# Kernel optimization log

Measured on AMD Instinct MI355X. Metric: run time of the kernel, lower is better.

The kernel has to match this reference:

```python
import jax, jax.numpy as jnp
import numpy as np

BATCH, DIM, L, N = 2, 4096, 2048, 16


def setup_inputs() -> dict:
    key = jax.random.key(0)
    ks = jax.random.split(key, 8)
    ri = lambda k, shape: jax.random.randint(k, shape, -127, 128).astype(jnp.int32)
    return {
        "u": ri(ks[0], (BATCH, DIM, L)),
        "dt": ri(ks[1], (BATCH, DIM, L)),
        "B": ri(ks[2], (BATCH, N, L)),
        "C": ri(ks[3], (BATCH, N, L)),
        "z": ri(ks[4], (BATCH, DIM, L)),
        "A_log": ri(ks[5], (DIM, N)),
        "D": ri(ks[6], (DIM,)),
        "dt_bias": ri(ks[7], (DIM,)),
        # per-tensor absmax-style scales (scalar fp32 buffers in QSScan)
        "u_scale": jnp.float32(0.01),
        "dt_scale": jnp.float32(0.004),
        "A_scale": jnp.float32(0.02),
        "B_scale": jnp.float32(0.02),
        "C_scale": jnp.float32(0.02),
        "z_scale": jnp.float32(0.02),
        "D_scale": jnp.float32(0.01),
        "dt_bias_scale": jnp.float32(0.02),
    }


def reference(u, dt, B, C, z, A_log, D, dt_bias,
              u_scale, dt_scale, A_scale, B_scale, C_scale,
              z_scale, D_scale, dt_bias_scale):
    # Dequantize INT8 operands (fused in the CUDA kernel)
    u_f = u.astype(jnp.float32) * u_scale                         # [b,d,l]
    delta = dt.astype(jnp.float32) * dt_scale \
        + (dt_bias.astype(jnp.float32) * dt_bias_scale)[None, :, None]
    delta = jax.nn.softplus(delta)                                # delta_softplus=True
    A = -jnp.exp(A_log.astype(jnp.float32) * A_scale)             # [d,n]
    B_f = B.astype(jnp.float32) * B_scale                         # [b,n,l]
    C_f = C.astype(jnp.float32) * C_scale                         # [b,n,l]

    # time-major inputs for the sequential scan
    xs = (jnp.moveaxis(delta, -1, 0),   # [l,b,d]
          jnp.moveaxis(u_f, -1, 0),     # [l,b,d]
          jnp.moveaxis(B_f, -1, 0),     # [l,b,n]
          jnp.moveaxis(C_f, -1, 0))     # [l,b,n]
    x0 = jnp.zeros((u.shape[0], u.shape[1], A.shape[1]), jnp.float32)  # [b,d,n]

    def step(x, ins):
        d_t, u_t, b_t, c_t = ins
        dA = jnp.exp(d_t[..., None] * A)                          # [b,d,n]
        x = dA * x + (d_t * u_t)[..., None] * b_t[:, None, :]     # ZOH-style discretization
        y_t = jnp.einsum('bdn,bn->bd', x, c_t)
        return x, y_t

    _, ys = jax.lax.scan(step, x0, xs)                            # [l,b,d]
    y = jnp.moveaxis(ys, 0, -1)                                   # [b,d,l]
    y = y + (D.astype(jnp.float32) * D_scale)[None, :, None] * u_f
    z_f = z.astype(jnp.float32) * z_scale
    return y * z_f * jax.nn.sigmoid(z_f)                          # gate: y * silu(z)
```

## Files before the change

### kernel.cpp

```cpp
#include <hip/hip_runtime.h>


#define LOG2E 1.44269504088896340736f
#define LN2F  0.69314718055994530942f

constexpr int BATCH = 2;
constexpr int DIM   = 4096;
constexpr int LSEQ  = 2048;
constexpr int NST   = 16;
constexpr int SCANS = BATCH * DIM;
constexpr int K     = 64;
constexpr int LC    = LSEQ / K;
constexpr int SPB   = 256;
constexpr int NSG   = SCANS / SPB;

__device__ __forceinline__ float softplus_f(float x) {
    float e = __builtin_amdgcn_exp2f(x * LOG2E);
    return __builtin_amdgcn_logf(1.f + e) * LN2F;
}

__device__ __forceinline__ int pack8(int4 v) {
    return (v.x & 255) | ((v.y & 255) << 8) | ((v.z & 255) << 16) | ((v.w & 255) << 24);
}

#define LOAD_A2()                                                              \
    float A2[NST];                                                             \
    {                                                                          \
        const int4* ap = (const int4*)(A_log + d * NST);                       \
        int4 a0 = ap[0], a1 = ap[1], a2 = ap[2], a3 = ap[3];                   \
        const int ai[NST] = {a0.x,a0.y,a0.z,a0.w, a1.x,a1.y,a1.z,a1.w,         \
                             a2.x,a2.y,a2.z,a2.w, a3.x,a3.y,a3.z,a3.w};        \
        _Pragma("unroll")                                                      \
        for (int n = 0; n < NST; ++n)                                          \
            A2[n] = -__builtin_amdgcn_exp2f((float)ai[n] * (A_s * LOG2E)) * LOG2E; \
    }

#define STEP4(q, bt, ct)                                                       \
    {                                                                          \
        const float4 Bq = *(const float4*)((bt) + 4 * (q));                    \
        const float4 Cq = *(const float4*)((ct) + 4 * (q));                    \
        x[4*(q)+0] = __builtin_fmaf(__builtin_amdgcn_exp2f(A2[4*(q)+0] * delta), x[4*(q)+0], w * Bq.x); \
        y = __builtin_fmaf(x[4*(q)+0], Cq.x, y);                               \
        x[4*(q)+1] = __builtin_fmaf(__builtin_amdgcn_exp2f(A2[4*(q)+1] * delta), x[4*(q)+1], w * Bq.y); \
        y = __builtin_fmaf(x[4*(q)+1], Cq.y, y);                               \
        x[4*(q)+2] = __builtin_fmaf(__builtin_amdgcn_exp2f(A2[4*(q)+2] * delta), x[4*(q)+2], w * Bq.z); \
        y = __builtin_fmaf(x[4*(q)+2], Cq.z, y);                               \
        x[4*(q)+3] = __builtin_fmaf(__builtin_amdgcn_exp2f(A2[4*(q)+3] * delta), x[4*(q)+3], w * Bq.w); \
        y = __builtin_fmaf(x[4*(q)+3], Cq.w, y);                               \
    }

#define STEP4B(q, bt)                                                          \
    {                                                                          \
        const float4 Bq = *(const float4*)((bt) + 4 * (q));                    \
        x[4*(q)+0] = __builtin_fmaf(__builtin_amdgcn_exp2f(A2[4*(q)+0] * delta), x[4*(q)+0], w * Bq.x); \
        x[4*(q)+1] = __builtin_fmaf(__builtin_amdgcn_exp2f(A2[4*(q)+1] * delta), x[4*(q)+1], w * Bq.y); \
        x[4*(q)+2] = __builtin_fmaf(__builtin_amdgcn_exp2f(A2[4*(q)+2] * delta), x[4*(q)+2], w * Bq.z); \
        x[4*(q)+3] = __builtin_fmaf(__builtin_amdgcn_exp2f(A2[4*(q)+3] * delta), x[4*(q)+3], w * Bq.w); \
    }

__global__ __launch_bounds__(256, 4) void qs_phase1(
    const int* __restrict__ u,  const int* __restrict__ dt,
    const int* __restrict__ Bm, const int* __restrict__ A_log,
    const int* __restrict__ dt_bias,
    const float* __restrict__ u_sp, const float* __restrict__ dt_sp,
    const float* __restrict__ A_sp, const float* __restrict__ B_sp,
    const float* __restrict__ dtb_sp,
    float* __restrict__ Sbuf, float* __restrict__ Xbuf)
{
    const int tid = threadIdx.x;
    const int cg  = blockIdx.x >> 5;
    const int sg  = blockIdx.x & 31;
    const int scan = sg * SPB + tid;
    const int d  = scan & (DIM - 1);
    const int bb = sg >> 4;

    __shared__ int   sud[256 * 17];
    __shared__ float tB[LC * 20];

    const float u_s = *u_sp, dt_s = *dt_sp, A_s = *A_sp, B_s = *B_sp, dtb_s = *dtb_sp;
    LOAD_A2();
    const float dtb = (float)dt_bias[d] * dtb_s;

    const int lc8 = tid >> 3, lo8 = tid & 7;
    const int in0 = sg * SPB * LSEQ + cg * LC;
    const int kB  = tid & 31, nB0 = tid >> 5;
    const int bcol = tid * 68;

#pragma unroll
    for (int p = 0; p < 8; ++p) {
        const int col = p * 32 + lc8;
        const int ga  = in0 + col * LSEQ + 4 * lo8;
        sud[col * 17 + lo8]     = pack8(*(const int4*)(u  + ga));
        sud[col * 17 + 8 + lo8] = pack8(*(const int4*)(dt + ga));
    }
#pragma unroll
    for (int j2 = 0; j2 < 2; ++j2) {
        const int n = nB0 + 8 * j2;
        tB[kB * 20 + n] = (float)Bm[(bb * NST + n) * LSEQ + cg * LC + kB];
    }
    __syncthreads();

    float x[NST];
#pragma unroll
    for (int n = 0; n < NST; ++n) x[n] = 0.f;
    float S = 0.f;

    const signed char* sc = (const signed char*)sud;
#pragma unroll 4
    for (int k = 0; k < LC; ++k) {
        const float uf    = (float)sc[bcol + k] * u_s;
        const float delta = softplus_f((float)sc[bcol + 32 + k] * dt_s + dtb);
        const float w     = delta * uf * B_s;
        S += delta;
        const float* bt = &tB[k * 20];
        STEP4B(0, bt); STEP4B(1, bt); STEP4B(2, bt); STEP4B(3, bt);
    }

    Sbuf[cg * SCANS + scan] = S;
    float4* Xo = (float4*)(Xbuf + (cg * SCANS + scan) * NST);
#pragma unroll
    for (int q = 0; q < 4; ++q)
        Xo[q] = make_float4(x[4*q], x[4*q+1], x[4*q+2], x[4*q+3]);
}

__global__ __launch_bounds__(256) void qs_combine(
    const int* __restrict__ A_log, const float* __restrict__ A_sp,
    const float* __restrict__ Sbuf, float* __restrict__ Xbuf)
{
    const int idx  = blockIdx.x * 256 + threadIdx.x;
    const int scan = idx >> 4, n = idx & 15;
    const int d    = scan & (DIM - 1);
    const float A2 = -__builtin_amdgcn_exp2f(
        (float)A_log[d * NST + n] * ((*A_sp) * LOG2E)) * LOG2E;
    float x = 0.f;
#pragma unroll 8
    for (int c = 0; c < K; ++c) {
        const int off = c * (SCANS * NST) + idx;
        const float Xe = Xbuf[off];
        const float P  = __builtin_amdgcn_exp2f(A2 * Sbuf[c * SCANS + scan]);
        Xbuf[off] = x;
        x = __builtin_fmaf(P, x, Xe);
    }
}

__global__ __launch_bounds__(256, 4) void qs_phase2(
    const int* __restrict__ u,  const int* __restrict__ dt,
    const int* __restrict__ Bm, const int* __restrict__ Cm,
    const int* __restrict__ z,  const int* __restrict__ A_log,
    const int* __restrict__ Dv, const int* __restrict__ dt_bias,
    const float* __restrict__ u_sp,  const float* __restrict__ dt_sp,
    const float* __restrict__ A_sp,  const float* __restrict__ B_sp,
    const float* __restrict__ C_sp,  const float* __restrict__ z_sp,
    const float* __restrict__ D_sp,  const float* __restrict__ dtb_sp,
    const float* __restrict__ XI, float* __restrict__ out)
{
    const int tid = threadIdx.x;
    const int cg  = blockIdx.x >> 5;
    const int sg  = blockIdx.x & 31;
    const int scan = sg * SPB + tid;
    const int d  = scan & (DIM - 1);
    const int bb = sg >> 4;

    __shared__ int   suz[256 * 25];
    __shared__ float tB[LC * 20];
    __shared__ float tC[LC * 20];

    const float u_s = *u_sp, dt_s = *dt_sp, A_s = *A_sp, B_s = *B_sp;
    const float C_s = *C_sp, z_s  = *z_sp,  D_s = *D_sp, dtb_s = *dtb_sp;
    LOAD_A2();
    const float dtb = (float)dt_bias[d] * dtb_s;
    const float Dd  = (float)Dv[d] * D_s;

    float x[NST];
    {
        const float4* xi = (const float4*)(XI + (cg * SCANS + scan) * NST);
        const float4 x0 = xi[0], x1 = xi[1], x2 = xi[2], x3 = xi[3];
        x[0]=x0.x; x[1]=x0.y; x[2]=x0.z; x[3]=x0.w;
        x[4]=x1.x; x[5]=x1.y; x[6]=x1.z; x[7]=x1.w;
        x[8]=x2.x; x[9]=x2.y; x[10]=x2.z; x[11]=x2.w;
        x[12]=x3.x; x[13]=x3.y; x[14]=x3.z; x[15]=x3.w;
    }

    const int lc8 = tid >> 3, lo8 = tid & 7;
    const int in0 = sg * SPB * LSEQ + cg * LC;
    const int kB  = tid & 31, nB0 = tid >> 5;
    const int bcol = tid * 100;
    const int ob   = scan * LSEQ + cg * LC;

#pragma unroll
    for (int p = 0; p < 8; ++p) {
        const int col = p * 32 + lc8;
        const int ga  = in0 + col * LSEQ + 4 * lo8;
        suz[col * 25 + lo8]      = pack8(*(const int4*)(u  + ga));
        suz[col * 25 + 8 + lo8]  = pack8(*(const int4*)(dt + ga));
        suz[col * 25 + 16 + lo8] = pack8(*(const int4*)(z  + ga));
    }
#pragma unroll
    for (int j2 = 0; j2 < 2; ++j2) {
        const int n  = nB0 + 8 * j2;
        const int gr = (bb * NST + n) * LSEQ + cg * LC + kB;
        tB[kB * 20 + n] = (float)Bm[gr];
        tC[kB * 20 + n] = (float)Cm[gr];
    }
    __syncthreads();

    const signed char* sc = (const signed char*)suz;
    float ya[16];
#pragma unroll 4
    for (int k = 0; k < LC; ++k) {
        const float uf    = (float)sc[bcol + k] * u_s;
        const float delta = softplus_f((float)sc[bcol + 32 + k] * dt_s + dtb);
        const float w     = delta * uf * B_s;
        const float zf    = (float)sc[bcol + 64 + k] * z_s;
        const float gate  = zf * __builtin_amdgcn_rcpf(
                                1.f + __builtin_amdgcn_exp2f(-zf * LOG2E));
        const float* bt = &tB[k * 20];
        const float* ct = &tC[k * 20];
        float y = 0.f;
        STEP4(0, bt, ct); STEP4(1, bt, ct); STEP4(2, bt, ct); STEP4(3, bt, ct);
        ya[k & 15] = __builtin_fmaf(y, C_s, Dd * uf) * gate;
        if ((k & 15) == 15) {
            float* ob2 = out + ob + (k - 15);
#pragma unroll
            for (int q = 0; q < 4; ++q)
                *(float4*)(ob2 + 4 * q) =
                    make_float4(ya[4*q], ya[4*q+1], ya[4*q+2], ya[4*q+3]);
        }
    }
}

extern "C" void kernel_launch(void* const* d_in, const int* in_sizes, int n_in,
                              void* d_out, int out_size, void* d_ws, size_t ws_size,
                              hipStream_t stream) {
    const int* u   = (const int*)d_in[0];
    const int* dt  = (const int*)d_in[1];
    const int* Bm  = (const int*)d_in[2];
    const int* Cm  = (const int*)d_in[3];
    const int* z   = (const int*)d_in[4];
    const int* Al  = (const int*)d_in[5];
    const int* Dv  = (const int*)d_in[6];
    const int* dtb = (const int*)d_in[7];
    const float* u_sp = (const float*)d_in[8],  * dt_sp = (const float*)d_in[9];
    const float* A_sp = (const float*)d_in[10], * B_sp  = (const float*)d_in[11];
    const float* C_sp = (const float*)d_in[12], * z_sp  = (const float*)d_in[13];
    const float* D_sp = (const float*)d_in[14], * dtb_sp= (const float*)d_in[15];

    float* Xbuf = (float*)d_ws;
    float* Sbuf = Xbuf + (size_t)K * SCANS * NST;

    dim3 blk(256);
    qs_phase1<<<dim3(K * NSG), blk, 0, stream>>>(u, dt, Bm, Al, dtb,
        u_sp, dt_sp, A_sp, B_sp, dtb_sp, Sbuf, Xbuf);
    qs_combine<<<dim3(SCANS * NST / 256), blk, 0, stream>>>(Al, A_sp, Sbuf, Xbuf);
    qs_phase2<<<dim3(K * NSG), blk, 0, stream>>>(u, dt, Bm, Cm, z, Al, Dv, dtb,
        u_sp, dt_sp, A_sp, B_sp, C_sp, z_sp, D_sp, dtb_sp, Xbuf, (float*)d_out);
}
```

Measured before the change: 149.6 us.

## Pre-transpose B/C into time-major float buffer and read them via uniform global loads

Adds a prep kernel that converts B and C to float and interleaves them time-major, 32 floats per timestep, in workspace. The scan kernels then read B/C straight from this buffer with wave-uniform addresses (likely scalar or cached loads) instead of staging transposed tiles in LDS. The per-thread int8 unpack now reads one packed word per four timesteps and extracts bytes by shift, replacing per-byte LDS reads, and the inner loop is fully unrolled. The cost is an extra kernel launch and global/cache traffic for B/C inside the hot loop.

```diff
diff --git a/kernel.cpp b/kernel.cpp
--- a/kernel.cpp
+++ b/kernel.cpp
@@ -21,6 +21,10 @@
 
 __device__ __forceinline__ int pack8(int4 v) {
     return (v.x & 255) | ((v.y & 255) << 8) | ((v.z & 255) << 16) | ((v.w & 255) << 24);
+}
+
+__device__ __forceinline__ float sb(int w, int b) {
+    return (float)((signed char)(w >> (8 * b)));
 }
 
 #define LOAD_A2()                                                              \
@@ -35,10 +39,10 @@
             A2[n] = -__builtin_amdgcn_exp2f((float)ai[n] * (A_s * LOG2E)) * LOG2E; \
     }
 
-#define STEP4(q, bt, ct)                                                       \
+#define STEP4(q, bp)                                                           \
     {                                                                          \
-        const float4 Bq = *(const float4*)((bt) + 4 * (q));                    \
-        const float4 Cq = *(const float4*)((ct) + 4 * (q));                    \
+        const float4 Bq = *(const float4*)((bp) + 4 * (q));                    \
+        const float4 Cq = *(const float4*)((bp) + 16 + 4 * (q));               \
         x[4*(q)+0] = __builtin_fmaf(__builtin_amdgcn_exp2f(A2[4*(q)+0] * delta), x[4*(q)+0], w * Bq.x); \
         y = __builtin_fmaf(x[4*(q)+0], Cq.x, y);                               \
         x[4*(q)+1] = __builtin_fmaf(__builtin_amdgcn_exp2f(A2[4*(q)+1] * delta), x[4*(q)+1], w * Bq.y); \
@@ -49,18 +53,32 @@
         y = __builtin_fmaf(x[4*(q)+3], Cq.w, y);                               \
     }
 
-#define STEP4B(q, bt)                                                          \
+#define STEP4B(q, bp)                                                          \
     {                                                                          \
-        const float4 Bq = *(const float4*)((bt) + 4 * (q));                    \
+        const float4 Bq = *(const float4*)((bp) + 4 * (q));                    \
         x[4*(q)+0] = __builtin_fmaf(__builtin_amdgcn_exp2f(A2[4*(q)+0] * delta), x[4*(q)+0], w * Bq.x); \
         x[4*(q)+1] = __builtin_fmaf(__builtin_amdgcn_exp2f(A2[4*(q)+1] * delta), x[4*(q)+1], w * Bq.y); \
         x[4*(q)+2] = __builtin_fmaf(__builtin_amdgcn_exp2f(A2[4*(q)+2] * delta), x[4*(q)+2], w * Bq.z); \
         x[4*(q)+3] = __builtin_fmaf(__builtin_amdgcn_exp2f(A2[4*(q)+3] * delta), x[4*(q)+3], w * Bq.w); \
     }
 
+__global__ __launch_bounds__(256) void qs_prep(
+    const int* __restrict__ Bm, const int* __restrict__ Cm,
+    float* __restrict__ BCf)
+{
+    const int idx = blockIdx.x * 256 + threadIdx.x;
+    const int n   = idx & 15;
+    const int t   = (idx >> 4) & (LSEQ - 1);
+    const int bb  = idx >> 15;
+    const int src = (bb * NST + n) * LSEQ + t;
+    float* dst = BCf + ((size_t)(bb * LSEQ + t)) * 32;
+    dst[n]      = (float)Bm[src];
+    dst[16 + n] = (float)Cm[src];
+}
+
 __global__ __launch_bounds__(256, 4) void qs_phase1(
     const int* __restrict__ u,  const int* __restrict__ dt,
-    const int* __restrict__ Bm, const int* __restrict__ A_log,
+    const float* __restrict__ BCf, const int* __restrict__ A_log,
     const int* __restrict__ dt_bias,
     const float* __restrict__ u_sp, const float* __restrict__ dt_sp,
     const float* __restrict__ A_sp, const float* __restrict__ B_sp,
@@ -74,8 +92,7 @@
     const int d  = scan & (DIM - 1);
     const int bb = sg >> 4;
 
-    __shared__ int   sud[256 * 17];
-    __shared__ float tB[LC * 20];
+    __shared__ int sud[256 * 17];
 
     const float u_s = *u_sp, dt_s = *dt_sp, A_s = *A_sp, B_s = *B_sp, dtb_s = *dtb_sp;
     LOAD_A2();
@@ -83,8 +100,6 @@
 
     const int lc8 = tid >> 3, lo8 = tid & 7;
     const int in0 = sg * SPB * LSEQ + cg * LC;
-    const int kB  = tid & 31, nB0 = tid >> 5;
-    const int bcol = tid * 68;
 
 #pragma unroll
     for (int p = 0; p < 8; ++p) {
@@ -93,11 +108,6 @@
         sud[col * 17 + lo8]     = pack8(*(const int4*)(u  + ga));
         sud[col * 17 + 8 + lo8] = pack8(*(const int4*)(dt + ga));
     }
-#pragma unroll
-    for (int j2 = 0; j2 < 2; ++j2) {
-        const int n = nB0 + 8 * j2;
-        tB[kB * 20 + n] = (float)Bm[(bb * NST + n) * LSEQ + cg * LC + kB];
-    }
     __syncthreads();
 
     float x[NST];
@@ -105,15 +115,22 @@
     for (int n = 0; n < NST; ++n) x[n] = 0.f;
     float S = 0.f;
 
-    const signed char* sc = (const signed char*)sud;
-#pragma unroll 4
-    for (int k = 0; k < LC; ++k) {
-        const float uf    = (float)sc[bcol + k] * u_s;
-        const float delta = softplus_f((float)sc[bcol + 32 + k] * dt_s + dtb);
-        const float w     = delta * uf * B_s;
-        S += delta;
-        const float* bt = &tB[k * 20];
-        STEP4B(0, bt); STEP4B(1, bt); STEP4B(2, bt); STEP4B(3, bt);
+    const int* swp = &sud[tid * 17];
+    const float* bp0 = BCf + (size_t)(bb * LSEQ + cg * LC) * 32;
+#pragma unroll
+    for (int k4 = 0; k4 < 8; ++k4) {
+        const int uw = swp[k4];
+        const int dw = swp[8 + k4];
+#pragma unroll
+        for (int b = 0; b < 4; ++b) {
+            const int k = 4 * k4 + b;
+            const float uf    = sb(uw, b) * u_s;
+            const float delta = softplus_f(sb(dw, b) * dt_s + dtb);
+            const float w     = delta * uf * B_s;
+            S += delta;
+            const float* bp = bp0 + k * 32;
+            STEP4B(0, bp); STEP4B(1, bp); STEP4B(2, bp); STEP4B(3, bp);
+        }
     }
 
     Sbuf[cg * SCANS + scan] = S;
@@ -145,8 +162,8 @@
 
 __global__ __launch_bounds__(256, 4) void qs_phase2(
     const int* __restrict__ u,  const int* __restrict__ dt,
-    const int* __restrict__ Bm, const int* __restrict__ Cm,
-    const int* __restrict__ z,  const int* __restrict__ A_log,
+    const float* __restrict__ BCf, const int* __restrict__ z,
+    const int* __restrict__ A_log,
     const int* __restrict__ Dv, const int* __restrict__ dt_bias,
     const float* __restrict__ u_sp,  const float* __restrict__ dt_sp,
     const float* __restrict__ A_sp,  const float* __restrict__ B_sp,
@@ -161,9 +178,7 @@
     const int d  = scan & (DIM - 1);
     const int bb = sg >> 4;
 
-    __shared__ int   suz[256 * 25];
-    __shared__ float tB[LC * 20];
-    __shared__ float tC[LC * 20];
+    __shared__ int suz[256 * 25];
 
     const float u_s = *u_sp, dt_s = *dt_sp, A_s = *A_sp, B_s = *B_sp;
     const float C_s = *C_sp, z_s  = *z_sp,  D_s = *D_sp, dtb_s = *dtb_sp;
@@ -183,9 +198,7 @@
 
     const int lc8 = tid >> 3, lo8 = tid & 7;
     const int in0 = sg * SPB * LSEQ + cg * LC;
-    const int kB  = tid & 31, nB0 = tid >> 5;
-    const int bcol = tid * 100;
-    const int ob   = scan * LSEQ + cg * LC;
+    const int ob  = scan * LSEQ + cg * LC;
 
 #pragma unroll
     for (int p = 0; p < 8; ++p) {
@@ -195,36 +208,36 @@
         suz[col * 25 + 8 + lo8]  = pack8(*(const int4*)(dt + ga));
         suz[col * 25 + 16 + lo8] = pack8(*(const int4*)(z  + ga));
     }
-#pragma unroll
-    for (int j2 = 0; j2 < 2; ++j2) {
-        const int n  = nB0 + 8 * j2;
-        const int gr = (bb * NST + n) * LSEQ + cg * LC + kB;
-        tB[kB * 20 + n] = (float)Bm[gr];
-        tC[kB * 20 + n] = (float)Cm[gr];
-    }
     __syncthreads();
 
-    const signed char* sc = (const signed char*)suz;
+    const int* swp = &suz[tid * 25];
+    const float* bp0 = BCf + (size_t)(bb * LSEQ + cg * LC) * 32;
     float ya[16];
-#pragma unroll 4
-    for (int k = 0; k < LC; ++k) {
-        const float uf    = (float)sc[bcol + k] * u_s;
-        const float delta = softplus_f((float)sc[bcol + 32 + k] * dt_s + dtb);
-        const float w     = delta * uf * B_s;
-        const float zf    = (float)sc[bcol + 64 + k] * z_s;
-        const float gate  = zf * __builtin_amdgcn_rcpf(
-                                1.f + __builtin_amdgcn_exp2f(-zf * LOG2E));
-        const float* bt = &tB[k * 20];
-        const float* ct = &tC[k * 20];
-        float y = 0.f;
-        STEP4(0, bt, ct); STEP4(1, bt, ct); STEP4(2, bt, ct); STEP4(3, bt, ct);
-        ya[k & 15] = __builtin_fmaf(y, C_s, Dd * uf) * gate;
-        if ((k & 15) == 15) {
-            float* ob2 = out + ob + (k - 15);
-#pragma unroll
-            for (int q = 0; q < 4; ++q)
-                *(float4*)(ob2 + 4 * q) =
-                    make_float4(ya[4*q], ya[4*q+1], ya[4*q+2], ya[4*q+3]);
+#pragma unroll
+    for (int k4 = 0; k4 < 8; ++k4) {
+        const int uw = swp[k4];
+        const int dw = swp[8 + k4];
+        const int zw = swp[16 + k4];
+#pragma unroll
+        for (int b = 0; b < 4; ++b) {
+            const int k = 4 * k4 + b;
+            const float uf    = sb(uw, b) * u_s;
+            const float delta = softplus_f(sb(dw, b) * dt_s + dtb);
+            const float w     = delta * uf * B_s;
+            const float zf    = sb(zw, b) * z_s;
+            const float gate  = zf * __builtin_amdgcn_rcpf(
+                                    1.f + __builtin_amdgcn_exp2f(-zf * LOG2E));
+            const float* bp = bp0 + k * 32;
+            float y = 0.f;
+            STEP4(0, bp); STEP4(1, bp); STEP4(2, bp); STEP4(3, bp);
+            ya[k & 15] = __builtin_fmaf(y, C_s, Dd * uf) * gate;
+            if ((k & 15) == 15) {
+                float* ob2 = out + ob + (k - 15);
+#pragma unroll
+                for (int q = 0; q < 4; ++q)
+                    *(float4*)(ob2 + 4 * q) =
+                        make_float4(ya[4*q], ya[4*q+1], ya[4*q+2], ya[4*q+3]);
+            }
         }
     }
 }
@@ -247,11 +260,13 @@
 
     float* Xbuf = (float*)d_ws;
     float* Sbuf = Xbuf + (size_t)K * SCANS * NST;
+    float* BCf  = Sbuf + (size_t)K * SCANS;
 
     dim3 blk(256);
-    qs_phase1<<<dim3(K * NSG), blk, 0, stream>>>(u, dt, Bm, Al, dtb,
+    qs_prep<<<dim3(BATCH * LSEQ * NST / 256), blk, 0, stream>>>(Bm, Cm, BCf);
+    qs_phase1<<<dim3(K * NSG), blk, 0, stream>>>(u, dt, BCf, Al, dtb,
         u_sp, dt_sp, A_sp, B_sp, dtb_sp, Sbuf, Xbuf);
     qs_combine<<<dim3(SCANS * NST / 256), blk, 0, stream>>>(Al, A_sp, Sbuf, Xbuf);
-    qs_phase2<<<dim3(K * NSG), blk, 0, stream>>>(u, dt, Bm, Cm, z, Al, Dv, dtb,
+    qs_phase2<<<dim3(K * NSG), blk, 0, stream>>>(u, dt, BCf, z, Al, Dv, dtb,
         u_sp, dt_sp, A_sp, B_sp, C_sp, z_sp, D_sp, dtb_sp, Xbuf, (float*)d_out);
 }
```

After: 190.6 us. 27.4% more time.
